# Optimization experiments

Hardware: AMD Instinct MI355X
Metric: run time of the kernel (lower is better)

Reference implementation:

```python
import jax, jax.numpy as jnp
import numpy as np

NUM_HEADS = 16
ROPE_BASE = 10000.0


def _rope_cos_sin(T, head_dim, dtype):
    # standard rotary: angles[t, i] = t * base^(-2i/head_dim), half-split layout
    inv_freq = 1.0 / (ROPE_BASE ** (jnp.arange(0, head_dim, 2, dtype=jnp.float32) / head_dim))
    ang = jnp.arange(T, dtype=jnp.float32)[:, None] * inv_freq[None, :]  # [T, hd/2]
    cos = jnp.concatenate([jnp.cos(ang), jnp.cos(ang)], axis=-1).astype(dtype)  # [T, hd]
    sin = jnp.concatenate([jnp.sin(ang), jnp.sin(ang)], axis=-1).astype(dtype)
    return cos, sin


def _rotate_half(t):
    t1, t2 = jnp.split(t, 2, axis=-1)
    return jnp.concatenate([-t2, t1], axis=-1)


def _apply_rope(t, cos, sin):
    # t: [B, H, T, hd]; cos/sin: [T, hd]
    return t * cos[None, None] + _rotate_half(t) * sin[None, None]


def setup_inputs() -> dict:
    key = jax.random.key(0)
    B, T, C = 2, 2048, 1024
    k1, k2, k3 = jax.random.split(key, 3)
    x = jax.random.normal(k1, (B, T, C), dtype=jnp.float32)
    w_attn = jax.random.normal(k2, (C, 3 * C), dtype=jnp.float32) * (C ** -0.5)
    w_proj = jax.random.normal(k3, (C, C), dtype=jnp.float32) * (C ** -0.5)
    return {"x": x, "w_attn": w_attn, "w_proj": w_proj}


def reference(x, w_attn, w_proj):
    B, T, C = x.shape
    H = NUM_HEADS
    hd = C // H

    qkv = x @ w_attn  # [B, T, 3C]
    q, k, v = jnp.split(qkv, 3, axis=-1)
    # [B, T, C] -> [B, H, T, hd]
    q = q.reshape(B, T, H, hd).transpose(0, 2, 1, 3)
    k = k.reshape(B, T, H, hd).transpose(0, 2, 1, 3)
    v = v.reshape(B, T, H, hd).transpose(0, 2, 1, 3)

    cos, sin = _rope_cos_sin(T, hd, x.dtype)
    q = _apply_rope(q, cos, sin)
    k = _apply_rope(k, cos, sin)

    scale = 1.0 / np.sqrt(hd).astype(np.float32)
    att = jnp.einsum('bhqd,bhkd->bhqk', q, k) * scale  # [B, H, T, T]
    causal = jnp.tril(jnp.ones((T, T), dtype=bool))
    att = jnp.where(causal[None, None], att, jnp.array(-jnp.inf, dtype=att.dtype))
    att = jax.nn.softmax(att, axis=-1)
    y = jnp.einsum('bhqk,bhkd->bhqd', att, v)  # [B, H, T, hd]
    y = y.transpose(0, 2, 1, 3).reshape(B, T, C)
    return y @ w_proj
```

## Files before the change

kernel.cpp:

```cpp
#include <hip/hip_runtime.h>

typedef unsigned short u16;
typedef unsigned int u32;
typedef unsigned long long u64;
typedef __attribute__((ext_vector_type(8))) short s16x8;
typedef __attribute__((ext_vector_type(8))) __bf16 bf16x8;
typedef __attribute__((ext_vector_type(4))) float fx4;
typedef __attribute__((ext_vector_type(16))) float fx16;
typedef __attribute__((ext_vector_type(2))) u32 u32x2;
typedef __attribute__((ext_vector_type(4))) u32 u32x4;

__device__ __forceinline__ fx4 mfma_16x16x32(s16x8 a, s16x8 b, fx4 c) {
  return __builtin_amdgcn_mfma_f32_16x16x32_bf16(
      __builtin_bit_cast(bf16x8, a), __builtin_bit_cast(bf16x8, b), c, 0, 0, 0);
}
__device__ __forceinline__ fx16 mfma_32x32x16(s16x8 a, s16x8 b, fx16 c) {
  return __builtin_amdgcn_mfma_f32_32x32x16_bf16(
      __builtin_bit_cast(bf16x8, a), __builtin_bit_cast(bf16x8, b), c, 0, 0, 0);
}

__device__ __forceinline__ u16 f2bf(float f) {
  u32 u = __builtin_bit_cast(u32, f);
  u32 r = u + 0x7fffu + ((u >> 16) & 1u);
  return (u16)(r >> 16);
}
__device__ __forceinline__ float bf2f(u16 h) {
  u32 u = ((u32)h) << 16;
  return __builtin_bit_cast(float, u);
}

__device__ __forceinline__ u32 cvtpk(float lo, float hi) {
  u32 r;
  asm("v_cvt_pk_bf16_f32 %0, %1, %2" : "=v"(r) : "v"(lo), "v"(hi));
  return r;
}

__device__ __forceinline__ float max3f(float a, float b, float c) {
  float r;
  asm("v_max3_f32 %0, %1, %2, %3" : "=v"(r) : "v"(a), "v"(b), "v"(c));
  return r;
}

__device__ __forceinline__ void plswap(u32& x, u32& y) {
  typedef __attribute__((ext_vector_type(2))) unsigned int uix2;
  uix2 r = __builtin_amdgcn_permlane32_swap(x, y, false, false);
  x = r[0];
  y = r[1];
}

__device__ __forceinline__ float xhalf_max(float v) {
  u32 a = __builtin_bit_cast(u32, v), b = a;
  plswap(a, b);
  return fmaxf(__builtin_bit_cast(float, a), __builtin_bit_cast(float, b));
}
__device__ __forceinline__ float xhalf_sum(float v) {
  u32 a = __builtin_bit_cast(u32, v), b = a;
  plswap(a, b);
  return __builtin_bit_cast(float, a) + __builtin_bit_cast(float, b);
}

__device__ __forceinline__ void gload16(const void* g, void* l) {
  __builtin_amdgcn_global_load_lds(
      (const __attribute__((address_space(1))) u32*)g,
      (__attribute__((address_space(3))) u32*)l, 16, 0, 0);
}

#define B_ 2
#define T_ 2048
#define C_ 1024
#define H_ 16
#define HD_ 64
#define BH_ 32
#define M_ 4096
#define CF_ 0.18033688011112042f

__global__ __launch_bounds__(256) void prep_k(
    const float* __restrict__ x, const float* __restrict__ wa,
    const float* __restrict__ wp, u16* __restrict__ xb, u16* __restrict__ waT,
    u16* __restrict__ wpT, float* __restrict__ ct, float* __restrict__ st) {
  __shared__ u16 T_s[64 * 72];
  int b = blockIdx.x, tid = threadIdx.x;
  if (b < 2048) {
    int id = b * 256 + tid;
    const fx4* p = (const fx4*)(x + (u64)id * 8);
    fx4 v0 = p[0], v1 = p[1];
    s16x8 r;
#pragma unroll
    for (int j = 0; j < 4; ++j) {
      r[j] = (short)f2bf(v0[j]);
      r[4 + j] = (short)f2bf(v1[j]);
    }
    *((s16x8*)xb + id) = r;
  } else if (b < 3072) {
    const float* W;
    u16* WT;
    int Ncols, bx, by;
    if (b < 2816) {
      int i = b - 2048;
      W = wa; WT = waT; Ncols = 3072; bx = i % 48; by = i / 48;
    } else {
      int i = b - 2816;
      W = wp; WT = wpT; Ncols = 1024; bx = i % 16; by = i / 16;
    }
    int c0 = bx * 64, r0 = by * 64;
#pragma unroll
    for (int it = 0; it < 4; ++it) {
      int idx = it * 256 + tid;
      int r = idx >> 4, c4 = (idx & 15) * 4;
      fx4 v = *(const fx4*)(W + (u64)(r0 + r) * Ncols + c0 + c4);
#pragma unroll
      for (int j = 0; j < 4; ++j) T_s[(c4 + j) * 72 + r] = f2bf(v[j]);
    }
    __syncthreads();
#pragma unroll
    for (int it = 0; it < 2; ++it) {
      int idx = it * 256 + tid;
      int rc = idx >> 3, c8 = (idx & 7) * 8;
      s16x8 v = *(const s16x8*)(T_s + rc * 72 + c8);
      *(s16x8*)(WT + (u64)(c0 + rc) * 1024 + r0 + c8) = v;
    }
  } else {
    int id = (b - 3072) * 256 + tid;
    int t = id >> 5, i = id & 31;
    float f = exp2f(-(float)i * (13.287712379549449f / 32.0f));
    float a = (float)t * f;
    float s, c;
    sincosf(a, &s, &c);
    ct[id] = c;
    st[id] = s;
  }
}

template <int EPI>
__global__ __launch_bounds__(256, 3) void gemm_bt_k(
    const u16* __restrict__ A, const u16* __restrict__ B, float* __restrict__ C,
    u16* __restrict__ Qo, u16* __restrict__ Ko, u16* __restrict__ Vo,
    const float* __restrict__ ct, const float* __restrict__ st,
    int M, int N, int K) {
  __shared__ u16 AsS[3][128 * 32];
  __shared__ u16 BsS[3][128 * 32];
  int tid = threadIdx.x, lane = tid & 63, w = tid >> 6;
  int wm = w >> 1, wn = w & 1, l15 = lane & 15, l4 = lane >> 4;
  int nwg = gridDim.x * gridDim.y;
  int id = blockIdx.y * gridDim.x + blockIdx.x;
  int qq = nwg >> 3;
  id = (id & 7) * qq + (id >> 3);
  int m0 = (id / gridDim.x) * 128, n0 = (id % gridDim.x) * 128;
  fx4 acc[4][4] = {};

  const u16* asrc[2];
  const u16* bsrc[2];
#pragma unroll
  for (int g = 0; g < 2; ++g) {
    int idx = g * 256 + tid;
    int row = idx >> 2, slot = (idx & 3) ^ (row & 3);
    asrc[g] = A + (u64)(m0 + row) * K + slot * 8;
    bsrc[g] = B + (u64)(n0 + row) * K + slot * 8;
  }

#define GSTAGE(S, KOFF)                                                      \
  do {                                                                       \
    _Pragma("unroll")                                                        \
    for (int g_ = 0; g_ < 2; ++g_) {                                         \
      gload16(asrc[g_] + (KOFF), (char*)AsS[S] + g_ * 4096 + tid * 16);      \
      gload16(bsrc[g_] + (KOFF), (char*)BsS[S] + g_ * 4096 + tid * 16);      \
    }                                                                        \
  } while (0)

#define GCOMP(S)                                                             \
  do {                                                                       \
    s16x8 a_[4], b_[4];                                                      \
    _Pragma("unroll")                                                        \
    for (int mi_ = 0; mi_ < 4; ++mi_) {                                      \
      int r_ = wm * 64 + mi_ * 16 + l15;                                     \
      a_[mi_] = *(const s16x8*)((const char*)AsS[S] + r_ * 64 +              \
                                ((l4 ^ (r_ & 3)) * 16));                     \
    }                                                                        \
    _Pragma("unroll")                                                        \
    for (int ni_ = 0; ni_ < 4; ++ni_) {                                      \
      int r_ = wn * 64 + ni_ * 16 + l15;                                     \
      b_[ni_] = *(const s16x8*)((const char*)BsS[S] + r_ * 64 +              \
                                ((l4 ^ (r_ & 3)) * 16));                     \
    }                                                                        \
    _Pragma("unroll")                                                        \
    for (int mi_ = 0; mi_ < 4; ++mi_)                                        \
      _Pragma("unroll")                                                      \
      for (int ni_ = 0; ni_ < 4; ++ni_)                                      \
        acc[mi_][ni_] = mfma_16x16x32(a_[mi_], b_[ni_], acc[mi_][ni_]);      \
  } while (0)

  int NT = K >> 5;
  GSTAGE(0, 0);
  GSTAGE(1, 32);
  int s0 = 0, s1 = 1, s2 = 2;
  for (int t = 0; t < NT; ++t) {
    __builtin_amdgcn_s_barrier();
    __builtin_amdgcn_sched_barrier(0);
    if (t + 2 < NT) GSTAGE(s2, (t + 2) * 32);
    __builtin_amdgcn_sched_barrier(0);
    if (t < NT - 2)
      asm volatile("s_waitcnt vmcnt(8)" ::: "memory");
    else if (t == NT - 2)
      asm volatile("s_waitcnt vmcnt(4)" ::: "memory");
    else
      asm volatile("s_waitcnt vmcnt(0)" ::: "memory");
    __builtin_amdgcn_s_barrier();
    __builtin_amdgcn_sched_barrier(0);
    GCOMP(s0);
    int tmp = s0;
    s0 = s1;
    s1 = s2;
    s2 = tmp;
  }
#undef GSTAGE
#undef GCOMP

  if (EPI == 0) {
#pragma unroll
    for (int mi = 0; mi < 4; ++mi)
#pragma unroll
      for (int ni = 0; ni < 4; ++ni)
#pragma unroll
        for (int r = 0; r < 4; ++r) {
          u64 row = (u64)(m0 + wm * 64 + mi * 16 + l4 * 4 + r);
          int col = n0 + wn * 64 + ni * 16 + l15;
          C[row * N + col] = acc[mi][ni][r];
        }
  } else {
#pragma unroll
    for (int mi = 0; mi < 4; ++mi)
#pragma unroll
      for (int r = 0; r < 4; ++r) {
        int row = m0 + wm * 64 + mi * 16 + l4 * 4 + r;
        int b2 = row >> 11, t = row & (T_ - 1);
#pragma unroll
        for (int ni = 0; ni < 2; ++ni) {
          int col = n0 + wn * 64 + ni * 16 + l15;
          int qi = col >> 10, h = (col >> 6) & 15, d = ni * 16 + l15;
          float lo = acc[mi][ni][r], hi = acc[mi][ni + 2][r];
          if (qi == 2) {
            u64 vbase =
                ((((u64)(b2 * H_ + h)) * (T_ / 8) + (t >> 3)) * HD_ + d) * 8 + (t & 7);
            Vo[vbase] = f2bf(lo);
            Vo[vbase + 32 * 8] = f2bf(hi);
          } else {
            float c = ct[t * 32 + d], s = st[t * 32 + d];
            float sc = (qi == 0) ? CF_ : 1.0f;
            u16* dst = (qi == 0) ? Qo : Ko;
            u64 base = ((((u64)(b2 * H_ + h)) * 8 + (d >> 3)) * T_ + t) * 8 + (d & 7);
            dst[base] = f2bf((lo * c - hi * s) * sc);
            dst[base + (u64)4 * T_ * 8] = f2bf((hi * c + lo * s) * sc);
          }
        }
      }
  }
}


#define LOADK(KC, KVI)                                                 \
  do {                                                                 \
    _Pragma("unroll")                                                  \
    for (int ks_ = 0; ks_ < 4; ++ks_)                                  \
      KC[ks_] = *(const s16x8*)(kp[ks_] + (u64)(KVI) * 256);           \
  } while (0)

#define LOADV(VC, KVI)                                                 \
  do {                                                                 \
    const u16* vk_ = vpb + (u64)(KVI) * 2048;                          \
    VC[0] = *(const s16x8*)(vk_);                                      \
    VC[1] = *(const s16x8*)(vk_ + 256);                                \
    VC[2] = *(const s16x8*)(vk_ + 1024);                               \
    VC[3] = *(const s16x8*)(vk_ + 1280);                               \
  } while (0)

#define ATTN_STEP(KC, VC, KVI)                                                \
  do {                                                                        \
    fx16 s_ = {};                                                             \
    __builtin_amdgcn_s_setprio(1);                                            \
    _Pragma("unroll")                                                         \
    for (int ks_ = 0; ks_ < 4; ++ks_)                                         \
      s_ = mfma_32x32x16(KC[ks_], qf[ks_], s_);                               \
    __builtin_amdgcn_s_setprio(0);                                            \
    if ((KVI) == jt) {                                                        \
      _Pragma("unroll")                                                       \
      for (int r_ = 0; r_ < 16; ++r_) {                                       \
        int cr_ = (r_ & 3) + 8 * (r_ >> 2) + 4 * h;                           \
        s_[r_] = (cr_ > ql) ? -1e30f : s_[r_];                                \
      }                                                                       \
    }                                                                         \
    float u0_ = max3f(s_[0], s_[1], s_[2]);                                   \
    float u1_ = max3f(s_[3], s_[4], s_[5]);                                   \
    float u2_ = max3f(s_[6], s_[7], s_[8]);                                   \
    float u3_ = max3f(s_[9], s_[10], s_[11]);                                 \
    float u4_ = max3f(s_[12], s_[13], s_[14]);                                \
    float v0_ = max3f(u0_, u1_, s_[15]);                                      \
    float v1_ = max3f(u2_, u3_, u4_);                                         \
    float rowmax_ = xhalf_max(fmaxf(v0_, v1_));                               \
    if (!__all(rowmax_ <= m + 8.f)) {                                         \
      float mnew_ = fmaxf(m, rowmax_);                                        \
      float corr_ = exp2f(m - mnew_);                                         \
      l *= corr_;                                                             \
      oL *= corr_;                                                            \
      oH *= corr_;                                                            \
      m = mnew_;                                                              \
    }                                                                         \
    float p_[16];                                                             \
    _Pragma("unroll")                                                         \
    for (int r_ = 0; r_ < 16; ++r_) p_[r_] = exp2f(s_[r_] - m);               \
    float a0_ = (p_[0] + p_[8]) + (p_[1] + p_[9]);                            \
    float a1_ = (p_[2] + p_[10]) + (p_[3] + p_[11]);                          \
    float a2_ = (p_[4] + p_[12]) + (p_[5] + p_[13]);                          \
    float a3_ = (p_[6] + p_[14]) + (p_[7] + p_[15]);                          \
    l += xhalf_sum((a0_ + a1_) + (a2_ + a3_));                                \
    u32 x0_ = cvtpk(p_[0], p_[1]), x1_ = cvtpk(p_[2], p_[3]);                 \
    u32 y0_ = cvtpk(p_[4], p_[5]), y1_ = cvtpk(p_[6], p_[7]);                 \
    plswap(x0_, y0_);                                                         \
    plswap(x1_, y1_);                                                         \
    u32x4 f0w_ = {x0_, x1_, y0_, y1_};                                        \
    u32 x2_ = cvtpk(p_[8], p_[9]), x3_ = cvtpk(p_[10], p_[11]);               \
    u32 y2_ = cvtpk(p_[12], p_[13]), y3_ = cvtpk(p_[14], p_[15]);             \
    plswap(x2_, y2_);                                                         \
    plswap(x3_, y3_);                                                         \
    u32x4 f1w_ = {x2_, x3_, y2_, y3_};                                        \
    s16x8 pf0_ = __builtin_bit_cast(s16x8, f0w_);                             \
    s16x8 pf1_ = __builtin_bit_cast(s16x8, f1w_);                             \
    __builtin_amdgcn_s_setprio(1);                                            \
    oL = mfma_32x32x16(VC[0], pf0_, oL);                                      \
    oH = mfma_32x32x16(VC[1], pf0_, oH);                                      \
    oL = mfma_32x32x16(VC[2], pf1_, oL);                                      \
    oH = mfma_32x32x16(VC[3], pf1_, oH);                                      \
    __builtin_amdgcn_s_setprio(0);                                            \
  } while (0)

#define OSTRIDE 68

__global__ __launch_bounds__(256, 3) void attn_fwd_k(
    const u16* __restrict__ Qp, const u16* __restrict__ Kp,
    const u16* __restrict__ Vp, u16* __restrict__ Y) {
  __shared__ float Ob[4 * 32 * OSTRIDE];
  __shared__ float Ml[4 * 32 * 2];
  int tid = threadIdx.x, lane = tid & 63, w = tid >> 6;
  int ql = lane & 31, h = lane >> 5;
  int bh = blockIdx.x & 31;
  int jt = 63 - (blockIdx.x >> 5);
  int q0 = jt * 32;
  int b2 = bh >> 4, head = bh & 15;
  int n = jt + 1;
  int lo = (w * n) >> 2, hi = ((w + 1) * n) >> 2;

  s16x8 qf[4];
#pragma unroll
  for (int ks = 0; ks < 4; ++ks)
    qf[ks] = *(const s16x8*)(Qp + (((u64)bh * 8 + ks * 2 + h) * T_ + q0 + ql) * 8);

  const u16* kp[4];
#pragma unroll
  for (int ks = 0; ks < 4; ++ks)
    kp[ks] = Kp + (((u64)bh * 8 + ks * 2 + h) * T_ + ql) * 8;
  const u16* vpb = Vp + (((u64)bh * (T_ / 8) + h) * HD_ + ql) * 8;

  fx16 oL = {}, oH = {};
  float m = -1e30f, l = 0.f;

  if (lo < hi) {
    s16x8 kA[4], vA[4], kB[4], vB[4];
    LOADK(kA, lo);
    LOADV(vA, lo);
    int kv = lo;
    for (; kv + 1 < hi; kv += 2) {
      LOADK(kB, kv + 1);
      LOADV(vB, kv + 1);
      ATTN_STEP(kA, vA, kv);
      if (kv + 2 < hi) {
        LOADK(kA, kv + 2);
        LOADV(vA, kv + 2);
      }
      ATTN_STEP(kB, vB, kv + 1);
    }
    if (kv < hi) ATTN_STEP(kA, vA, kv);
  }

  {
    float* ob = Ob + (w * 32 + ql) * OSTRIDE;
#pragma unroll
    for (int g = 0; g < 4; ++g) {
      fx4 a = {oL[4 * g], oL[4 * g + 1], oL[4 * g + 2], oL[4 * g + 3]};
      *(fx4*)(ob + 8 * g + 4 * h) = a;
      fx4 b = {oH[4 * g], oH[4 * g + 1], oH[4 * g + 2], oH[4 * g + 3]};
      *(fx4*)(ob + 32 + 8 * g + 4 * h) = b;
    }
    if (h == 0) {
      Ml[(w * 32 + ql) * 2] = m;
      Ml[(w * 32 + ql) * 2 + 1] = l;
    }
  }
  __syncthreads();

  {
    int q = tid >> 3, db = tid & 7;
    float mm0 = Ml[(0 * 32 + q) * 2], ll0 = Ml[(0 * 32 + q) * 2 + 1];
    float mm1 = Ml[(1 * 32 + q) * 2], ll1 = Ml[(1 * 32 + q) * 2 + 1];
    float mm2 = Ml[(2 * 32 + q) * 2], ll2 = Ml[(2 * 32 + q) * 2 + 1];
    float mm3 = Ml[(3 * 32 + q) * 2], ll3 = Ml[(3 * 32 + q) * 2 + 1];
    float mo = fmaxf(fmaxf(mm0, mm1), fmaxf(mm2, mm3));
    float w0 = exp2f(mm0 - mo), w1 = exp2f(mm1 - mo);
    float w2 = exp2f(mm2 - mo), w3 = exp2f(mm3 - mo);
    float rl = 1.0f / (ll0 * w0 + ll1 * w1 + ll2 * w2 + ll3 * w3);
    w0 *= rl; w1 *= rl; w2 *= rl; w3 *= rl;
    const float* ob = Ob + q * OSTRIDE + db * 8;
    fx4 aa = {}, bb = {};
#pragma unroll
    for (int i = 0; i < 4; ++i) {
      float wi = (i == 0) ? w0 : (i == 1) ? w1 : (i == 2) ? w2 : w3;
      fx4 pa = *(const fx4*)(ob + i * 32 * OSTRIDE);
      fx4 pb = *(const fx4*)(ob + i * 32 * OSTRIDE + 4);
      aa += wi * pa;
      bb += wi * pb;
    }
    u32x4 ow;
    ow[0] = cvtpk(aa[0], aa[1]);
    ow[1] = cvtpk(aa[2], aa[3]);
    ow[2] = cvtpk(bb[0], bb[1]);
    ow[3] = cvtpk(bb[2], bb[3]);
    int t = q0 + q;
    *(u32x4*)(Y + ((u64)(b2 * T_ + t)) * C_ + head * HD_ + db * 8) = ow;
  }
}

extern "C" void kernel_launch(void* const* d_in, const int* in_sizes, int n_in,
                              void* d_out, int out_size, void* d_ws, size_t ws_size,
                              hipStream_t stream) {
  (void)in_sizes; (void)n_in; (void)out_size; (void)ws_size;
  const float* x = (const float*)d_in[0];
  const float* w_attn = (const float*)d_in[1];
  const float* w_proj = (const float*)d_in[2];
  float* out = (float*)d_out;

  u16* xb = (u16*)d_ws;
  u16* waT = xb + (u64)M_ * C_;
  u16* wpT = waT + (u64)3 * C_ * C_;
  u16* Qp = wpT + (u64)C_ * C_;
  u16* Kp = Qp + (u64)BH_ * T_ * HD_;
  u16* Vp = Kp + (u64)BH_ * T_ * HD_;
  float* ct = (float*)(Vp + (u64)BH_ * T_ * HD_);
  float* st = ct + T_ * 32;
  u16* yb = xb;

  prep_k<<<3328, 256, 0, stream>>>(x, w_attn, w_proj, xb, waT, wpT, ct, st);

  gemm_bt_k<1><<<dim3(24, 32), 256, 0, stream>>>(xb, waT, nullptr, Qp, Kp, Vp,
                                                 ct, st, M_, 3 * C_, C_);

  attn_fwd_k<<<2048, 256, 0, stream>>>(Qp, Kp, Vp, yb);

  gemm_bt_k<0><<<dim3(8, 32), 256, 0, stream>>>(yb, wpT, out, nullptr, nullptr,
                                                nullptr, nullptr, nullptr,
                                                M_, C_, C_);
}
```

Measured before the change: 111.7 us.

## Add dedicated 256x256-tile QKV GEMM kernel with 512 threads and double buffering

Replaces the templated 128x128 QKV projection GEMM with a specialised kernel that uses 256x256 output tiles, 8 waves, a K-step of 64 and a two-stage LDS double buffer with XOR swizzle. The RoPE/QKV scatter epilogue moves into this kernel, and the generic GEMM keeps only the plain fp32 store. Larger tiles raise arithmetic intensity and cut global loads for the 4096x3072x1024 GEMM. In exchange the grid drops to 192 blocks, which is below one block per CU on a 256-CU part, and register and LDS pressure per block rises.

```diff
diff --git a/kernel.cpp b/kernel.cpp
--- a/kernel.cpp
+++ b/kernel.cpp
@@ -131,11 +131,115 @@
   }
 }
 
-template <int EPI>
+__global__ __launch_bounds__(512, 2) void gemm1_k(
+    const u16* __restrict__ A, const u16* __restrict__ B,
+    u16* __restrict__ Qo, u16* __restrict__ Ko, u16* __restrict__ Vo,
+    const float* __restrict__ ct, const float* __restrict__ st) {
+  __shared__ u16 AsS[2][256 * 64];
+  __shared__ u16 BsS[2][256 * 64];
+  const int K = 1024;
+  int tid = threadIdx.x, lane = tid & 63, w = tid >> 6;
+  int wm = w >> 2, wn = w & 3, l15 = lane & 15, l4 = lane >> 4;
+  int id = blockIdx.y * 12 + blockIdx.x;
+  id = (id & 7) * 24 + (id >> 3);
+  int m0 = (id / 12) * 256, n0 = (id % 12) * 256;
+
+  const u16* asrc[4];
+  const u16* bsrc[4];
+  int pdst[4];
+#pragma unroll
+  for (int q = 0; q < 4; ++q) {
+    int p = w * 256 + q * 64 + lane;
+    int row = p >> 3, s = (p & 7) ^ (row & 7);
+    pdst[q] = p * 16;
+    asrc[q] = A + (u64)(m0 + row) * K + s * 8;
+    bsrc[q] = B + (u64)(n0 + row) * K + s * 8;
+  }
+
+#define G1STAGE(BUF, KOFF)                                              \
+  do {                                                                  \
+    _Pragma("unroll")                                                   \
+    for (int q_ = 0; q_ < 4; ++q_)                                      \
+      gload16(asrc[q_] + (KOFF), (char*)AsS[BUF] + pdst[q_]);           \
+    _Pragma("unroll")                                                   \
+    for (int q_ = 0; q_ < 4; ++q_)                                      \
+      gload16(bsrc[q_] + (KOFF), (char*)BsS[BUF] + pdst[q_]);           \
+  } while (0)
+
+  fx4 acc[8][4] = {};
+
+  G1STAGE(0, 0);
+  for (int t = 0; t < 16; ++t) {
+    __builtin_amdgcn_s_barrier();
+    __builtin_amdgcn_sched_barrier(0);
+    if (t + 1 < 16) {
+      G1STAGE((t + 1) & 1, (t + 1) * 64);
+      __builtin_amdgcn_sched_barrier(0);
+      asm volatile("s_waitcnt vmcnt(8)" ::: "memory");
+    } else {
+      asm volatile("s_waitcnt vmcnt(0)" ::: "memory");
+    }
+    __builtin_amdgcn_s_barrier();
+    __builtin_amdgcn_sched_barrier(0);
+    int buf = t & 1;
+    s16x8 bf[4][2];
+#pragma unroll
+    for (int nj = 0; nj < 4; ++nj)
+#pragma unroll
+      for (int ks = 0; ks < 2; ++ks) {
+        int rb = wn * 64 + nj * 16 + l15;
+        int sl = ks * 4 + l4;
+        bf[nj][ks] = *(const s16x8*)((const char*)BsS[buf] +
+                                     (rb * 8 + (sl ^ (rb & 7))) * 16);
+      }
+#pragma unroll
+    for (int mi = 0; mi < 8; ++mi) {
+      int ra = wm * 128 + mi * 16 + l15;
+      s16x8 a0 = *(const s16x8*)((const char*)AsS[buf] +
+                                 (ra * 8 + (l4 ^ (ra & 7))) * 16);
+      s16x8 a1 = *(const s16x8*)((const char*)AsS[buf] +
+                                 (ra * 8 + ((4 + l4) ^ (ra & 7))) * 16);
+      __builtin_amdgcn_s_setprio(1);
+#pragma unroll
+      for (int nj = 0; nj < 4; ++nj) {
+        acc[mi][nj] = mfma_16x16x32(a0, bf[nj][0], acc[mi][nj]);
+        acc[mi][nj] = mfma_16x16x32(a1, bf[nj][1], acc[mi][nj]);
+      }
+      __builtin_amdgcn_s_setprio(0);
+    }
+  }
+#undef G1STAGE
+
+#pragma unroll
+  for (int mi = 0; mi < 8; ++mi)
+#pragma unroll
+    for (int r = 0; r < 4; ++r) {
+      int row = m0 + wm * 128 + mi * 16 + l4 * 4 + r;
+      int b2 = row >> 11, t = row & (T_ - 1);
+#pragma unroll
+      for (int nj = 0; nj < 2; ++nj) {
+        int col = n0 + wn * 64 + nj * 16 + l15;
+        int qi = col >> 10, h = (col >> 6) & 15, d = nj * 16 + l15;
+        float lo = acc[mi][nj][r], hi = acc[mi][nj + 2][r];
+        if (qi == 2) {
+          u64 vbase =
+              ((((u64)(b2 * H_ + h)) * (T_ / 8) + (t >> 3)) * HD_ + d) * 8 + (t & 7);
+          Vo[vbase] = f2bf(lo);
+          Vo[vbase + 32 * 8] = f2bf(hi);
+        } else {
+          float c = ct[t * 32 + d], s = st[t * 32 + d];
+          float sc = (qi == 0) ? CF_ : 1.0f;
+          u16* dst = (qi == 0) ? Qo : Ko;
+          u64 base = ((((u64)(b2 * H_ + h)) * 8 + (d >> 3)) * T_ + t) * 8 + (d & 7);
+          dst[base] = f2bf((lo * c - hi * s) * sc);
+          dst[base + (u64)4 * T_ * 8] = f2bf((hi * c + lo * s) * sc);
+        }
+      }
+    }
+}
+
 __global__ __launch_bounds__(256, 3) void gemm_bt_k(
     const u16* __restrict__ A, const u16* __restrict__ B, float* __restrict__ C,
-    u16* __restrict__ Qo, u16* __restrict__ Ko, u16* __restrict__ Vo,
-    const float* __restrict__ ct, const float* __restrict__ st,
     int M, int N, int K) {
   __shared__ u16 AsS[3][128 * 32];
   __shared__ u16 BsS[3][128 * 32];
@@ -215,47 +319,17 @@
 #undef GSTAGE
 #undef GCOMP
 
-  if (EPI == 0) {
-#pragma unroll
-    for (int mi = 0; mi < 4; ++mi)
-#pragma unroll
-      for (int ni = 0; ni < 4; ++ni)
-#pragma unroll
-        for (int r = 0; r < 4; ++r) {
-          u64 row = (u64)(m0 + wm * 64 + mi * 16 + l4 * 4 + r);
-          int col = n0 + wn * 64 + ni * 16 + l15;
-          C[row * N + col] = acc[mi][ni][r];
-        }
-  } else {
-#pragma unroll
-    for (int mi = 0; mi < 4; ++mi)
+#pragma unroll
+  for (int mi = 0; mi < 4; ++mi)
+#pragma unroll
+    for (int ni = 0; ni < 4; ++ni)
 #pragma unroll
       for (int r = 0; r < 4; ++r) {
-        int row = m0 + wm * 64 + mi * 16 + l4 * 4 + r;
-        int b2 = row >> 11, t = row & (T_ - 1);
-#pragma unroll
-        for (int ni = 0; ni < 2; ++ni) {
-          int col = n0 + wn * 64 + ni * 16 + l15;
-          int qi = col >> 10, h = (col >> 6) & 15, d = ni * 16 + l15;
-          float lo = acc[mi][ni][r], hi = acc[mi][ni + 2][r];
-          if (qi == 2) {
-            u64 vbase =
-                ((((u64)(b2 * H_ + h)) * (T_ / 8) + (t >> 3)) * HD_ + d) * 8 + (t & 7);
-            Vo[vbase] = f2bf(lo);
-            Vo[vbase + 32 * 8] = f2bf(hi);
-          } else {
-            float c = ct[t * 32 + d], s = st[t * 32 + d];
-            float sc = (qi == 0) ? CF_ : 1.0f;
-            u16* dst = (qi == 0) ? Qo : Ko;
-            u64 base = ((((u64)(b2 * H_ + h)) * 8 + (d >> 3)) * T_ + t) * 8 + (d & 7);
-            dst[base] = f2bf((lo * c - hi * s) * sc);
-            dst[base + (u64)4 * T_ * 8] = f2bf((hi * c + lo * s) * sc);
-          }
-        }
+        u64 row = (u64)(m0 + wm * 64 + mi * 16 + l4 * 4 + r);
+        int col = n0 + wn * 64 + ni * 16 + l15;
+        C[row * N + col] = acc[mi][ni][r];
       }
-  }
-}
-
+}
 
 #define LOADK(KC, KVI)                                                 \
   do {                                                                 \
@@ -448,12 +522,9 @@
 
   prep_k<<<3328, 256, 0, stream>>>(x, w_attn, w_proj, xb, waT, wpT, ct, st);
 
-  gemm_bt_k<1><<<dim3(24, 32), 256, 0, stream>>>(xb, waT, nullptr, Qp, Kp, Vp,
-                                                 ct, st, M_, 3 * C_, C_);
+  gemm1_k<<<dim3(12, 16), 512, 0, stream>>>(xb, waT, Qp, Kp, Vp, ct, st);
 
   attn_fwd_k<<<2048, 256, 0, stream>>>(Qp, Kp, Vp, yb);
 
-  gemm_bt_k<0><<<dim3(8, 32), 256, 0, stream>>>(yb, wpT, out, nullptr, nullptr,
-                                                nullptr, nullptr, nullptr,
-                                                M_, C_, C_);
-}
+  gemm_bt_k<<<dim3(8, 32), 256, 0, stream>>>(yb, wpT, out, M_, C_, C_);
+}
```

Result: slower. 119.5 us (+7.0%).

## Use barrier-free per-wave LDS double-buffered GEMM for output projection

Applied to the files above, without the earlier changes.

Splits the templated GEMM into a QKV kernel and a separate output-projection kernel. In the new projection kernel each wave stages its own 64x32 A and B slices into a private, XOR-swizzled LDS region with double buffering. Because no wave reads another wave's data, workgroup barriers are removed. The cost is that each wave loads its tiles redundantly instead of sharing them across the block, which raises global and LDS traffic, and occupancy drops to 2 blocks per CU.

```diff
diff --git a/kernel.cpp b/kernel.cpp
--- a/kernel.cpp
+++ b/kernel.cpp
@@ -131,9 +131,8 @@
   }
 }
 
-template <int EPI>
-__global__ __launch_bounds__(256, 3) void gemm_bt_k(
-    const u16* __restrict__ A, const u16* __restrict__ B, float* __restrict__ C,
+__global__ __launch_bounds__(256, 3) void gemm1_k(
+    const u16* __restrict__ A, const u16* __restrict__ B,
     u16* __restrict__ Qo, u16* __restrict__ Ko, u16* __restrict__ Vo,
     const float* __restrict__ ct, const float* __restrict__ st,
     int M, int N, int K) {
@@ -215,47 +214,118 @@
 #undef GSTAGE
 #undef GCOMP
 
-  if (EPI == 0) {
-#pragma unroll
-    for (int mi = 0; mi < 4; ++mi)
-#pragma unroll
-      for (int ni = 0; ni < 4; ++ni)
-#pragma unroll
-        for (int r = 0; r < 4; ++r) {
-          u64 row = (u64)(m0 + wm * 64 + mi * 16 + l4 * 4 + r);
-          int col = n0 + wn * 64 + ni * 16 + l15;
-          C[row * N + col] = acc[mi][ni][r];
-        }
-  } else {
-#pragma unroll
-    for (int mi = 0; mi < 4; ++mi)
-#pragma unroll
-      for (int r = 0; r < 4; ++r) {
-        int row = m0 + wm * 64 + mi * 16 + l4 * 4 + r;
-        int b2 = row >> 11, t = row & (T_ - 1);
-#pragma unroll
-        for (int ni = 0; ni < 2; ++ni) {
-          int col = n0 + wn * 64 + ni * 16 + l15;
-          int qi = col >> 10, h = (col >> 6) & 15, d = ni * 16 + l15;
-          float lo = acc[mi][ni][r], hi = acc[mi][ni + 2][r];
-          if (qi == 2) {
-            u64 vbase =
-                ((((u64)(b2 * H_ + h)) * (T_ / 8) + (t >> 3)) * HD_ + d) * 8 + (t & 7);
-            Vo[vbase] = f2bf(lo);
-            Vo[vbase + 32 * 8] = f2bf(hi);
-          } else {
-            float c = ct[t * 32 + d], s = st[t * 32 + d];
-            float sc = (qi == 0) ? CF_ : 1.0f;
-            u16* dst = (qi == 0) ? Qo : Ko;
-            u64 base = ((((u64)(b2 * H_ + h)) * 8 + (d >> 3)) * T_ + t) * 8 + (d & 7);
-            dst[base] = f2bf((lo * c - hi * s) * sc);
-            dst[base + (u64)4 * T_ * 8] = f2bf((hi * c + lo * s) * sc);
-          }
+#pragma unroll
+  for (int mi = 0; mi < 4; ++mi)
+#pragma unroll
+    for (int r = 0; r < 4; ++r) {
+      int row = m0 + wm * 64 + mi * 16 + l4 * 4 + r;
+      int b2 = row >> 11, t = row & (T_ - 1);
+#pragma unroll
+      for (int ni = 0; ni < 2; ++ni) {
+        int col = n0 + wn * 64 + ni * 16 + l15;
+        int qi = col >> 10, h = (col >> 6) & 15, d = ni * 16 + l15;
+        float lo = acc[mi][ni][r], hi = acc[mi][ni + 2][r];
+        if (qi == 2) {
+          u64 vbase =
+              ((((u64)(b2 * H_ + h)) * (T_ / 8) + (t >> 3)) * HD_ + d) * 8 + (t & 7);
+          Vo[vbase] = f2bf(lo);
+          Vo[vbase + 32 * 8] = f2bf(hi);
+        } else {
+          float c = ct[t * 32 + d], s = st[t * 32 + d];
+          float sc = (qi == 0) ? CF_ : 1.0f;
+          u16* dst = (qi == 0) ? Qo : Ko;
+          u64 base = ((((u64)(b2 * H_ + h)) * 8 + (d >> 3)) * T_ + t) * 8 + (d & 7);
+          dst[base] = f2bf((lo * c - hi * s) * sc);
+          dst[base + (u64)4 * T_ * 8] = f2bf((hi * c + lo * s) * sc);
         }
       }
-  }
-}
-
+    }
+}
+
+__global__ __launch_bounds__(256, 2) void gemm2_nb(
+    const u16* __restrict__ A, const u16* __restrict__ B, float* __restrict__ C,
+    int M, int N, int K) {
+  __shared__ u16 lds[4][2][2][64 * 32];
+  int tid = threadIdx.x, lane = tid & 63, w = tid >> 6;
+  int wm = w >> 1, wn = w & 1, l15 = lane & 15, l4 = lane >> 4;
+  int nwg = gridDim.x * gridDim.y;
+  int id = blockIdx.y * gridDim.x + blockIdx.x;
+  int qq = nwg >> 3;
+  id = (id & 7) * qq + (id >> 3);
+  int m0 = (id / gridDim.x) * 128 + wm * 64;
+  int n0 = (id % gridDim.x) * 128 + wn * 64;
+  fx4 acc[4][4] = {};
+
+  const u16* asrc[4];
+  const u16* bsrc[4];
+  int doff[4];
+#pragma unroll
+  for (int g = 0; g < 4; ++g) {
+    int p = g * 64 + lane;
+    int row = p >> 2, slot = (p & 3) ^ (row & 3);
+    doff[g] = p * 16;
+    asrc[g] = A + (u64)(m0 + row) * K + slot * 8;
+    bsrc[g] = B + (u64)(n0 + row) * K + slot * 8;
+  }
+
+#define STG(BUF, KOFF)                                                       \
+  do {                                                                       \
+    _Pragma("unroll")                                                        \
+    for (int g_ = 0; g_ < 4; ++g_) {                                         \
+      gload16(asrc[g_] + (KOFF), (char*)lds[w][BUF][0] + doff[g_]);          \
+      gload16(bsrc[g_] + (KOFF), (char*)lds[w][BUF][1] + doff[g_]);          \
+    }                                                                        \
+  } while (0)
+
+#define CMP(BUF)                                                             \
+  do {                                                                       \
+    s16x8 a_[4], b_[4];                                                      \
+    _Pragma("unroll")                                                        \
+    for (int mi_ = 0; mi_ < 4; ++mi_) {                                      \
+      int r_ = mi_ * 16 + l15;                                               \
+      a_[mi_] = *(const s16x8*)((const char*)lds[w][BUF][0] + r_ * 64 +      \
+                                ((l4 ^ (r_ & 3)) * 16));                     \
+    }                                                                        \
+    _Pragma("unroll")                                                        \
+    for (int ni_ = 0; ni_ < 4; ++ni_) {                                      \
+      int r_ = ni_ * 16 + l15;                                               \
+      b_[ni_] = *(const s16x8*)((const char*)lds[w][BUF][1] + r_ * 64 +      \
+                                ((l4 ^ (r_ & 3)) * 16));                     \
+    }                                                                        \
+    _Pragma("unroll")                                                        \
+    for (int mi_ = 0; mi_ < 4; ++mi_)                                        \
+      _Pragma("unroll")                                                      \
+      for (int ni_ = 0; ni_ < 4; ++ni_)                                      \
+        acc[mi_][ni_] = mfma_16x16x32(a_[mi_], b_[ni_], acc[mi_][ni_]);      \
+  } while (0)
+
+  int NT = K >> 5;
+  STG(0, 0);
+  for (int t = 0; t < NT; ++t) {
+    __builtin_amdgcn_sched_barrier(0);
+    if (t + 1 < NT) {
+      STG((t + 1) & 1, (t + 1) * 32);
+      asm volatile("s_waitcnt vmcnt(8)" ::: "memory");
+    } else {
+      asm volatile("s_waitcnt vmcnt(0)" ::: "memory");
+    }
+    __builtin_amdgcn_sched_barrier(0);
+    CMP(t & 1);
+  }
+#undef STG
+#undef CMP
+
+#pragma unroll
+  for (int mi = 0; mi < 4; ++mi)
+#pragma unroll
+    for (int ni = 0; ni < 4; ++ni)
+#pragma unroll
+      for (int r = 0; r < 4; ++r) {
+        u64 row = (u64)(m0 + mi * 16 + l4 * 4 + r);
+        int col = n0 + ni * 16 + l15;
+        C[row * N + col] = acc[mi][ni][r];
+      }
+}
 
 #define LOADK(KC, KVI)                                                 \
   do {                                                                 \
@@ -448,12 +518,10 @@
 
   prep_k<<<3328, 256, 0, stream>>>(x, w_attn, w_proj, xb, waT, wpT, ct, st);
 
-  gemm_bt_k<1><<<dim3(24, 32), 256, 0, stream>>>(xb, waT, nullptr, Qp, Kp, Vp,
-                                                 ct, st, M_, 3 * C_, C_);
+  gemm1_k<<<dim3(24, 32), 256, 0, stream>>>(xb, waT, Qp, Kp, Vp,
+                                            ct, st, M_, 3 * C_, C_);
 
   attn_fwd_k<<<2048, 256, 0, stream>>>(Qp, Kp, Vp, yb);
 
-  gemm_bt_k<0><<<dim3(8, 32), 256, 0, stream>>>(yb, wpT, out, nullptr, nullptr,
-                                                nullptr, nullptr, nullptr,
-                                                M_, C_, C_);
-}
+  gemm2_nb<<<dim3(8, 32), 256, 0, stream>>>(yb, wpT, out, M_, C_, C_);
+}
```

Result: faster. 104.8 us (-6.2%).
